# Performance work log

Hardware: AMD Instinct MI355X
Metric: run time of the kernel (lower is better)

Reference implementation:

```python
import jax, jax.numpy as jnp
import numpy as np
from jax import lax

B, C, H, W = 256, 64, 48, 48   # batch, in_channels, spatial_dim, spatial_dim
E = 5                           # num_experts (ConditionalConv2D default)
DIM = 64 + 1                    # n_regulators + 1


def setup_inputs() -> dict:
    key = jax.random.key(0)
    ks = jax.random.split(key, 24)
    def n(k, shape, s=0.05):
        return jax.random.normal(k, shape, jnp.float32) * s
    inp = {
        "spatial_maps": jax.random.normal(ks[0], (B, C, H, W), jnp.float32),
        "cluster_info": jax.random.randint(ks[1], (B,), 0, C),
        # ConditionalConv2D (1x1, num_experts=5)
        "expert_w": n(ks[2], (E, C, C)),          # [experts, out_c, in_c] (1x1 squeezed)
        "cond_b": n(ks[3], (C,)),
        "route_emb": n(ks[4], (C, 4 * C)),        # Embedding(num_clusters=C, pool_emb=4C)
        "route_W": n(ks[5], (E, 8 * C)),          # Linear(2*pool_emb -> E)
        "route_b": n(ks[6], (E,)),
        # weight-normed conv stack (v, g, bias, prelu-a)
        "v1": n(ks[7], (32, C, 3, 3)),  "g1": jnp.ones((32,), jnp.float32),  "cb1": n(ks[8], (32,)),  "a1": jnp.array(0.1, jnp.float32),
        "v2": n(ks[9], (64, 32, 3, 3)), "g2": jnp.ones((64,), jnp.float32),  "cb2": n(ks[10], (64,)), "a2": jnp.array(0.1, jnp.float32),
        "v3": n(ks[11], (128, 64, 3, 3)), "g3": jnp.ones((128,), jnp.float32), "cb3": n(ks[12], (128,)), "a3": jnp.array(0.1, jnp.float32),
        # cluster embedding + alpha + MLP
        "emb2": n(ks[13], (C, 128)),
        "alpha": jnp.array(1.0, jnp.float32),
        "mW1": n(ks[14], (64, 128)), "mb1": n(ks[15], (64,)), "a4": jnp.array(0.1, jnp.float32),
        "mW2": n(ks[16], (32, 64)),  "mb2": n(ks[17], (32,)), "a5": jnp.array(0.1, jnp.float32),
        "mW3": n(ks[18], (DIM, 32)), "mb3": n(ks[19], (DIM,)),
    }
    return inp


def _wn(v, g):
    # weight_norm over all dims except 0 (torch default dim=0)
    nrm = jnp.sqrt((v * v).sum((1, 2, 3)))
    return v * (g / nrm)[:, None, None, None]


def _conv(x, w, b):
    y = lax.conv_general_dilated(x, w, (1, 1), 'SAME',
                                 dimension_numbers=('NCHW', 'OIHW', 'NCHW'))
    return y + b[None, :, None, None]


def _prelu(x, a):
    return jnp.where(x >= 0, x, a * x)


def _mpool(x):
    return lax.reduce_window(x, -jnp.inf, lax.max, (1, 1, 2, 2), (1, 1, 2, 2), 'VALID')


def reference(spatial_maps, cluster_info, expert_w, cond_b, route_emb, route_W, route_b,
              v1, g1, cb1, a1, v2, g2, cb2, a2, v3, g3, cb3, a3,
              emb2, alpha, mW1, mb1, a4, mW2, mb2, a5, mW3, mb3):
    x = spatial_maps
    # routing: adaptive avg pool (2,2), flatten, concat cluster embedding, linear, sigmoid
    pooled = x.reshape(B, C, 2, H // 2, 2, W // 2).mean((3, 5)).reshape(B, 4 * C)
    feat = jnp.concatenate([pooled, route_emb[cluster_info]], axis=1)      # [B, 8C]
    rw = jax.nn.sigmoid(feat @ route_W.T + route_b)                        # [B, E]
    # per-sample expert-mixed 1x1 kernel, applied as batched 1x1 conv
    kern = jnp.einsum('be,eoi->boi', rw, expert_w)                         # [B, C, C]
    cc = jnp.einsum('boi,bihw->bohw', kern, x) + cond_b[None, :, None, None]
    out = jax.nn.sigmoid(cc) * x                                           # attention gate
    # dense conv stack
    h = _mpool(_prelu(_conv(out, _wn(v1, g1), cb1), a1))
    h = _mpool(_prelu(_conv(h, _wn(v2, g2), cb2), a2))
    h = _mpool(_prelu(_conv(h, _wn(v3, g3), cb3), a3))
    h = h.mean((2, 3))                                                      # AdaptiveAvgPool2d(1)+Flatten -> [B,128]
    h = h + emb2[cluster_info] * alpha
    # MLP head
    h = _prelu(h @ mW1.T + mb1, a4)
    h = _prelu(h @ mW2.T + mb2, a5)
    return h @ mW3.T + mb3                                                  # [B, DIM]
```

## Files before the change

kernel.cpp:

```cpp
#include <hip/hip_runtime.h>


typedef _Float16 f16;
typedef f16 f16x8 __attribute__((ext_vector_type(8)));
typedef f16 f16x4 __attribute__((ext_vector_type(4)));
typedef f16 f16x2 __attribute__((ext_vector_type(2)));
typedef __fp16 h16x2 __attribute__((ext_vector_type(2)));
typedef float f32x4 __attribute__((ext_vector_type(4)));

constexpr size_t OFF_POOLED = 0;
constexpr size_t OFF_KERN   = 65536;
constexpr size_t OFF_W1     = 65536 + 1048576;
constexpr size_t OFF_W2     = OFF_W1 + 32*64*12;
constexpr size_t OFF_W3     = OFF_W2 + 64*32*12;
constexpr size_t OFF_H1     = OFF_W3 + 128*64*12;

__device__ __forceinline__ float sigmoidf_(float z) {
    return __builtin_amdgcn_rcpf(1.0f + __expf(-z));
}

__device__ __forceinline__ f16x2 pkrtz(float a, float b) {
    h16x2 r = __builtin_amdgcn_cvt_pkrtz(a, b);
    f16x2 o; o[0] = (f16)r[0]; o[1] = (f16)r[1];
    return o;
}

__device__ __forceinline__ void store_slot8(f16* glds, int row, int sc, int icg, const float* c) {
    f16x2 p0 = pkrtz(c[0], c[1]);
    f16x2 p1 = pkrtz(c[2], c[3]);
    f16x2 p2 = pkrtz(c[4], c[5]);
    f16x2 p3 = pkrtz(c[6], c[7]);
    f16x8 hv = { p0[0], p0[1], p1[0], p1[1], p2[0], p2[1], p3[0], p3[1] };
    *(f16x8*)&glds[(row * 50 + sc) * 64 + ((icg ^ (sc & 7)) << 3)] = hv;
}

__global__ void k_wnorm(const float* __restrict__ v1, const float* __restrict__ g1,
                        const float* __restrict__ v2, const float* __restrict__ g2,
                        const float* __restrict__ v3, const float* __restrict__ g3,
                        float* __restrict__ ws)
{
    int bo = blockIdx.x;
    const float* v; const float* g; int IC, oc; int which;
    if (bo < 32)       { v = v1; g = g1; oc = bo;      IC = 64; which = 1; }
    else if (bo < 96)  { v = v2; g = g2; oc = bo - 32; IC = 32; which = 2; }
    else               { v = v3; g = g3; oc = bo - 96; IC = 64; which = 3; }
    int n = IC * 9;
    const float* vo = v + (size_t)oc * n;
    float s = 0.0f;
    for (int i = threadIdx.x; i < n; i += 256) { float xv = vo[i]; s += xv * xv; }
    __shared__ float swarp[4];
    __shared__ float sscale;
    int lane = threadIdx.x & 63, wid = threadIdx.x >> 6;
    #pragma unroll
    for (int off = 32; off; off >>= 1) s += __shfl_down(s, off);
    if (lane == 0) swarp[wid] = s;
    __syncthreads();
    if (threadIdx.x == 0) {
        float tsum = swarp[0] + swarp[1] + swarp[2] + swarp[3];
        sscale = g[oc] / sqrtf(tsum);
    }
    __syncthreads();
    float sc = sscale;
    if (which == 1) {
        f16* o1 = (f16*)(ws + OFF_W1);
        for (int i = threadIdx.x; i < n; i += 256) {
            int ic = i / 9, kk = i - ic * 9;
            o1[kk * 2048 + oc * 64 + (ic ^ ((oc & 7) << 3))] = (f16)(vo[i] * sc);
        }
    } else if (which == 2) {
        f16* o2 = (f16*)(ws + OFF_W2);
        for (int i = threadIdx.x; i < n; i += 256) {
            int ic = i / 9, kk = i - ic * 9;
            o2[(kk * 64 + oc) * 32 + ic] = (f16)(vo[i] * sc);
        }
    } else {
        f16* o3 = (f16*)(ws + OFF_W3);
        for (int i = threadIdx.x; i < n; i += 256) {
            int ic = i / 9, kk = i - ic * 9;
            o3[(kk * 128 + oc) * 64 + ic] = (f16)(vo[i] * sc);
        }
    }
}

__global__ void __launch_bounds__(64)
k_pool(const float* __restrict__ x, float* __restrict__ ws)
{
    int bc = blockIdx.x;
    int lane = threadIdx.x;
    const float4* p = (const float4*)(x + (size_t)bc * 2304);
    float a0 = 0.f, a1 = 0.f, a2 = 0.f, a3 = 0.f;
    #pragma unroll
    for (int j = 0; j < 9; j++) {
        int i = lane + 64 * j;
        int row = i / 12, cg = i - 12 * row;
        float4 v = p[i];
        float s = v.x + v.y + v.z + v.w;
        bool hq = (row >= 24), wq = (cg >= 6);
        a0 += (!hq && !wq) ? s : 0.f;
        a1 += (!hq &&  wq) ? s : 0.f;
        a2 += ( hq && !wq) ? s : 0.f;
        a3 += ( hq &&  wq) ? s : 0.f;
    }
    #pragma unroll
    for (int off = 32; off; off >>= 1) {
        a0 += __shfl_down(a0, off);
        a1 += __shfl_down(a1, off);
        a2 += __shfl_down(a2, off);
        a3 += __shfl_down(a3, off);
    }
    if (lane == 0) {
        int b = bc >> 6, c = bc & 63;
        float* d = ws + OFF_POOLED + (size_t)b * 256 + c * 4;
        d[0] = a0 * (1.0f / 576.0f);
        d[1] = a1 * (1.0f / 576.0f);
        d[2] = a2 * (1.0f / 576.0f);
        d[3] = a3 * (1.0f / 576.0f);
    }
}

__global__ void k_route(const int* __restrict__ cluster,
                        const float* __restrict__ route_emb,
                        const float* __restrict__ route_W,
                        const float* __restrict__ route_b,
                        const float* __restrict__ expert_w,
                        float* __restrict__ ws)
{
    int b = blockIdx.x, t = threadIdx.x;
    __shared__ float feat[512];
    __shared__ float rwv[5];
    __shared__ float red[256];
    int cl = cluster[b];
    feat[t]       = ws[OFF_POOLED + (size_t)b * 256 + t];
    feat[256 + t] = route_emb[(size_t)cl * 256 + t];
    __syncthreads();
    float f0 = feat[t], f1 = feat[256 + t];
    for (int e = 0; e < 5; e++) {
        float pv = f0 * route_W[e * 512 + t] + f1 * route_W[e * 512 + 256 + t];
        red[t] = pv;
        __syncthreads();
        if (t < 128) red[t] += red[t + 128];
        __syncthreads();
        if (t < 64) {
            float s = red[t] + red[t + 64];
            #pragma unroll
            for (int off = 32; off; off >>= 1) s += __shfl_down(s, off);
            if (t == 0) rwv[e] = 1.0f / (1.0f + __expf(-(s + route_b[e])));
        }
        __syncthreads();
    }
    float r0 = rwv[0], r1 = rwv[1], r2 = rwv[2], r3 = rwv[3], r4 = rwv[4];
    f16* khg = (f16*)(ws + OFF_KERN);
    for (int j = t; j < 4096; j += 256) {
        int oc = j >> 6, ic = j & 63;
        float kv = r0 * expert_w[j] + r1 * expert_w[4096 + j] +
                   r2 * expert_w[2 * 4096 + j] + r3 * expert_w[3 * 4096 + j] +
                   r4 * expert_w[4 * 4096 + j];
        khg[(size_t)b * 4096 + oc * 64 + (ic ^ ((oc & 7) << 3))] = (f16)kv;
    }
}

__global__ void __launch_bounds__(512, 4)
k_f1(const float* __restrict__ x, const f16* __restrict__ kernH,
     const float* __restrict__ cond_b, const f16* __restrict__ w1H,
     const float* __restrict__ cb1, const float* __restrict__ a1,
     f16* __restrict__ h1h)
{
    extern __shared__ char smem[];
    f16*  glds  = (f16*)smem;
    f16*  kh    = (f16*)(smem + 64000);
    float* cbl  = (float*)(smem + 72192);
    f16*  hm    = (f16*)smem;
    f16*  poolt = (f16*)(smem + 16384);

    const int t = threadIdx.x;
    const int tile = blockIdx.x;
    const int b = blockIdx.y;
    const int r0 = tile * 8;
    const int w = t >> 6, l = t & 63;
    const int l15 = l & 15, agrp = l >> 4;

    ((uint4*)kh)[t] = ((const uint4*)(kernH + (size_t)b * 4096))[t];
    if (t < 64) cbl[t] = cond_b[t];
    if (t < 160) {
        int row = t >> 4, rem = t & 15;
        int col = (rem >= 8) ? 49 : 0;
        int slot = rem & 7;
        uint4 z = {};
        *(uint4*)&glds[(row * 50 + col) * 64 + slot * 8] = z;
    }
    for (int e = t; e < 960; e += 512) {
        int row = e / 96;
        int rem = e - row * 96;
        int colg = rem >> 3;
        int icg = rem & 7;
        int r_in = r0 - 1 + row;
        float4 va[8];
        if (r_in >= 0 && r_in < 48) {
            const float4* xp = (const float4*)x + ((size_t)(b * 64 + icg * 8)) * 576 + r_in * 12 + colg;
            #pragma unroll
            for (int i = 0; i < 8; i++) va[i] = xp[i * 576];
        } else {
            #pragma unroll
            for (int i = 0; i < 8; i++) va[i] = (float4){0.f, 0.f, 0.f, 0.f};
        }
        float c0[8], c1[8], c2c[8], c3[8];
        #pragma unroll
        for (int i = 0; i < 8; i++) { c0[i] = va[i].x; c1[i] = va[i].y; c2c[i] = va[i].z; c3[i] = va[i].w; }
        int scb = colg * 4 + 1;
        store_slot8(glds, row, scb + 0, icg, c0);
        store_slot8(glds, row, scb + 1, icg, c1);
        store_slot8(glds, row, scb + 2, icg, c2c);
        store_slot8(glds, row, scb + 3, icg, c3);
    }
    __syncthreads();

    {
        const int nt0 = (w < 6) ? 4 * w : 24 + 3 * (w - 6);
        const int NT  = (w < 6) ? 4 : 3;
        f32x4 acc[4][4] = {};
        int srA[4], scA[4];
        #pragma unroll
        for (int j = 0; j < 4; j++) {
            int ntc = nt0 + ((j < NT) ? j : 0);
            int p = ntc * 16 + l15;
            srA[j] = p / 48; scA[j] = p - 48 * srA[j] + 1;
        }
        #pragma unroll
        for (int ks = 0; ks < 2; ks++) {
            f16x8 kfr[4];
            #pragma unroll
            for (int mt = 0; mt < 4; mt++) {
                int oc = mt * 16 + l15;
                kfr[mt] = *(const f16x8*)&kh[oc * 64 + (((ks * 4 + agrp) ^ (oc & 7)) << 3)];
            }
            #pragma unroll
            for (int j = 0; j < 4; j++) {
                f16x8 bfr = *(const f16x8*)&glds[(srA[j] * 50 + scA[j]) * 64 +
                                                 (((ks * 4 + agrp) ^ (scA[j] & 7)) << 3)];
                #pragma unroll
                for (int mt = 0; mt < 4; mt++)
                    acc[mt][j] = __builtin_amdgcn_mfma_f32_16x16x32_f16(kfr[mt], bfr, acc[mt][j], 0, 0, 0);
            }
        }
        f32x4 cbv[4];
        #pragma unroll
        for (int mt = 0; mt < 4; mt++) cbv[mt] = *(const f32x4*)&cbl[mt * 16 + 4 * agrp];
        #pragma unroll
        for (int j = 0; j < 4; j++) {
            if (j < NT) {
                int base = (srA[j] * 50 + scA[j]) * 64;
                int sw8 = (scA[j] & 7) << 3;
                #pragma unroll
                for (int mt = 0; mt < 4; mt++) {
                    int oc0 = mt * 16 + 4 * agrp;
                    int addr = base + (oc0 ^ sw8);
                    f16x4 xv4 = *(const f16x4*)&glds[addr];
                    float s0 = sigmoidf_(acc[mt][j][0] + cbv[mt][0]);
                    float s1 = sigmoidf_(acc[mt][j][1] + cbv[mt][1]);
                    float s2 = sigmoidf_(acc[mt][j][2] + cbv[mt][2]);
                    float s3 = sigmoidf_(acc[mt][j][3] + cbv[mt][3]);
                    f16x2 slo = pkrtz(s0, s1);
                    f16x2 shi = pkrtz(s2, s3);
                    f16x2 xlo = { xv4[0], xv4[1] };
                    f16x2 xhi = { xv4[2], xv4[3] };
                    f16x2 glo = slo * xlo;
                    f16x2 ghi = shi * xhi;
                    f16x4 g4 = { glo[0], glo[1], ghi[0], ghi[1] };
                    *(f16x4*)&glds[addr] = g4;
                }
            }
        }
    }
    __syncthreads();

    f32x4 c2[3][2] = {};
    {
        const int q = w;
        #pragma unroll
        for (int kt = 0; kt < 18; kt++) {
            const int kk = kt >> 1, hh = kt & 1;
            const int dy = kk / 3, dx = kk - dy * 3;
            f16x8 bfr2[2];
            #pragma unroll
            for (int nt = 0; nt < 2; nt++) {
                int oc = nt * 16 + l15;
                int slot = (hh * 4 + agrp) ^ (oc & 7);
                bfr2[nt] = *(const f16x8*)&w1H[(kk * 32 + oc) * 64 + slot * 8];
            }
            #pragma unroll
            for (int mtl = 0; mtl < 3; mtl++) {
                int sc = mtl * 16 + l15 + dx;
                int slot = (hh * 4 + agrp) ^ (sc & 7);
                f16x8 af = *(const f16x8*)&glds[((q + dy) * 50 + sc) * 64 + slot * 8];
                c2[mtl][0] = __builtin_amdgcn_mfma_f32_16x16x32_f16(af, bfr2[0], c2[mtl][0], 0, 0, 0);
                c2[mtl][1] = __builtin_amdgcn_mfma_f32_16x16x32_f16(af, bfr2[1], c2[mtl][1], 0, 0, 0);
            }
        }
    }
    __syncthreads();

    {
        const int q = w;
        #pragma unroll
        for (int mtl = 0; mtl < 3; mtl++)
            #pragma unroll
            for (int nt = 0; nt < 2; nt++) {
                float h0 = fmaxf(c2[mtl][nt][0], c2[mtl][nt][1]);
                float h1 = fmaxf(c2[mtl][nt][2], c2[mtl][nt][3]);
                f16x2 hp = pkrtz(h0, h1);
                int oc = nt * 16 + l15;
                int pp = mtl * 8 + 2 * agrp;
                *(f16x2*)&hm[(q * 32 + oc) * 26 + pp] = hp;
            }
    }
    __syncthreads();

    {
        const float av = a1[0];
        #pragma unroll
        for (int k = 0; k < 6; k++) {
            int e = t + 512 * k;
            int oc = e & 31, pos2 = e >> 5;
            int pr = pos2 / 24, pc = pos2 - 24 * pr;
            float v0 = (float)hm[((2 * pr) * 32 + oc) * 26 + pc];
            float v1 = (float)hm[((2 * pr + 1) * 32 + oc) * 26 + pc];
            float v = fmaxf(v0, v1) + cb1[oc];
            v = (v >= 0.0f) ? v : av * v;
            poolt[pos2 * 40 + oc] = (f16)v;
        }
    }
    __syncthreads();

    if (t < 384) {
        int pos2 = t >> 2, slot = t & 3;
        uint4 val = *(const uint4*)&poolt[pos2 * 40 + slot * 8];
        ((uint4*)h1h)[((size_t)b * 576 + tile * 96 + pos2) * 4 + slot] = val;
    }
}

__global__ void __launch_bounds__(512, 1)
k_f23(const f16* __restrict__ h1h, const f16* __restrict__ w2h,
      const float* __restrict__ cb2, const float* __restrict__ a2,
      const f16* __restrict__ w3h, const float* __restrict__ cb3, const float* __restrict__ a3,
      const int* __restrict__ cluster, const float* __restrict__ emb2, const float* __restrict__ alpha,
      const float* __restrict__ mW1, const float* __restrict__ mb1, const float* __restrict__ a4,
      const float* __restrict__ mW2, const float* __restrict__ mb2, const float* __restrict__ a5,
      const float* __restrict__ mW3, const float* __restrict__ mb3,
      float* __restrict__ out)
{
    extern __shared__ char smem[];
    f16*  x2    = (f16*)smem;
    f16*  h2l   = (f16*)(smem + 82944);
    float* ps   = (float*)(smem + 111168);
    float* hb   = (float*)(smem + 113216);
    float* t1   = (float*)(smem + 113728);
    float* t2   = (float*)(smem + 113984);
    f16*  dump2 = (f16*)smem;
    f16*  dump3 = (f16*)smem;

    const int b = blockIdx.x, t = threadIdx.x;
    const int w = t >> 6, l = t & 63;
    const int l15 = l & 15, agrp = l >> 4;

    for (int e = t; e < 400; e += 512) {
        int bp = e >> 2, slot = e & 3;
        int r, c;
        if (bp < 26)      { r = 0;  c = bp; }
        else if (bp < 52) { r = 25; c = bp - 26; }
        else if (bp < 76) { r = bp - 52 + 1; c = 0; }
        else              { r = bp - 76 + 1; c = 25; }
        uint4 z = {};
        *(uint4*)&x2[(r * 26 + c) * 40 + slot * 8] = z;
    }
    for (int e = t; e < 416; e += 512) {
        int bp = e >> 3, slot = e & 7;
        int r, c;
        if (bp < 14)      { r = 0;  c = bp; }
        else if (bp < 28) { r = 13; c = bp - 14; }
        else if (bp < 40) { r = bp - 28 + 1; c = 0; }
        else              { r = bp - 40 + 1; c = 13; }
        uint4 z = {};
        *(uint4*)&h2l[(r * 14 + c) * 72 + slot * 8] = z;
    }
    {
        const uint4* src = (const uint4*)(h1h + (size_t)b * 18432);
        for (int e = t; e < 2304; e += 512) {
            int pos = e >> 2, slot = e & 3;
            int r = pos / 24, c = pos - 24 * r;
            *(uint4*)&x2[((r + 1) * 26 + (c + 1)) * 40 + slot * 8] = src[e];
        }
    }
    __syncthreads();

    const int m = w & 3, half = w >> 2;
    f32x4 acc[18];
    {
        f16x8 afr[9];
        #pragma unroll
        for (int kk = 0; kk < 9; kk++)
            afr[kk] = *(const f16x8*)&w2h[(kk * 64 + m * 16 + l15) * 32 + agrp * 8];
        #pragma unroll
        for (int nt = 0; nt < 18; nt++) acc[nt] = (f32x4){0.f, 0.f, 0.f, 0.f};
        constexpr int K2[9] = {0, 40, 80, 26 * 40, 27 * 40, 28 * 40, 52 * 40, 53 * 40, 54 * 40};
        #pragma unroll
        for (int nt = 0; nt < 18; nt++) {
            int p = (half * 18 + nt) * 16 + l15;
            int r = p / 24, c = p - 24 * r;
            int base = (r * 26 + c) * 40 + agrp * 8;
            #pragma unroll
            for (int kk = 0; kk < 9; kk++) {
                f16x8 bfr = *(const f16x8*)&x2[base + K2[kk]];
                acc[nt] = __builtin_amdgcn_mfma_f32_16x16x32_f16(afr[kk], bfr, acc[nt], 0, 0, 0);
            }
        }
    }
    __syncthreads();

    #pragma unroll
    for (int nt = 0; nt < 18; nt++) {
        int p = (half * 18 + nt) * 16 + l15;
        f16x2 d0 = pkrtz(acc[nt][0], acc[nt][1]);
        f16x2 d1 = pkrtz(acc[nt][2], acc[nt][3]);
        f16x4 hv = { d0[0], d0[1], d1[0], d1[1] };
        *(f16x4*)&dump2[p * 72 + m * 16 + 4 * agrp] = hv;
    }
    __syncthreads();

    {
        const float a2v = a2[0];
        for (int e = t; e < 9216; e += 512) {
            int oc = e & 63, pos2 = e >> 6;
            int pr = pos2 / 12, pc = pos2 - 12 * pr;
            int p0 = (2 * pr) * 24 + 2 * pc;
            float mm = fmaxf(fmaxf((float)dump2[p0 * 72 + oc], (float)dump2[(p0 + 1) * 72 + oc]),
                             fmaxf((float)dump2[(p0 + 24) * 72 + oc], (float)dump2[(p0 + 25) * 72 + oc]));
            float v = mm + cb2[oc];
            v = (v >= 0.0f) ? v : a2v * v;
            h2l[((pr + 1) * 14 + (pc + 1)) * 72 + oc] = (f16)v;
        }
    }
    __syncthreads();

    f32x4 acc9[9];
    {
        int pb[9];
        #pragma unroll
        for (int nt = 0; nt < 9; nt++) {
            int p = nt * 16 + l15;
            int r = p / 12, c = p - 12 * r;
            pb[nt] = (r * 14 + c) * 72 + agrp * 8;
            acc9[nt] = (f32x4){0.f, 0.f, 0.f, 0.f};
        }
        constexpr int K3[9] = {0, 72, 144, 14 * 72, 15 * 72, 16 * 72, 28 * 72, 29 * 72, 30 * 72};
        #pragma unroll
        for (int kk = 0; kk < 9; kk++) {
            #pragma unroll
            for (int ks = 0; ks < 2; ks++) {
                f16x8 afr = *(const f16x8*)&w3h[(size_t)(kk * 128 + w * 16 + l15) * 64 + ks * 32 + agrp * 8];
                #pragma unroll
                for (int nt = 0; nt < 9; nt++) {
                    f16x8 bfr = *(const f16x8*)&h2l[pb[nt] + ks * 32 + K3[kk]];
                    acc9[nt] = __builtin_amdgcn_mfma_f32_16x16x32_f16(afr, bfr, acc9[nt], 0, 0, 0);
                }
            }
        }
    }
    #pragma unroll
    for (int nt = 0; nt < 9; nt++) {
        int p = nt * 16 + l15;
        f16x2 d0 = pkrtz(acc9[nt][0], acc9[nt][1]);
        f16x2 d1 = pkrtz(acc9[nt][2], acc9[nt][3]);
        f16x4 hv = { d0[0], d0[1], d1[0], d1[1] };
        *(f16x4*)&dump3[p * 136 + w * 16 + 4 * agrp] = hv;
    }
    __syncthreads();

    {
        int oc = t >> 2, q = t & 3;
        int qr = q >> 1, qc = q & 1;
        const float a3v = a3[0];
        float cbv = cb3[oc];
        float s = 0.f;
        #pragma unroll
        for (int i = 0; i < 3; i++)
            #pragma unroll
            for (int j = 0; j < 3; j++) {
                int pr = 3 * qr + i, pc = 3 * qc + j;
                int p0 = (2 * pr) * 12 + 2 * pc;
                float mm = fmaxf(fmaxf((float)dump3[p0 * 136 + oc], (float)dump3[(p0 + 1) * 136 + oc]),
                                 fmaxf((float)dump3[(p0 + 12) * 136 + oc], (float)dump3[(p0 + 13) * 136 + oc]));
                float v = mm + cbv;
                v = (v >= 0.0f) ? v : a3v * v;
                s += v;
            }
        ps[t] = s;
    }
    __syncthreads();
    if (t < 128) {
        int cl = cluster[b];
        hb[t] = (ps[4 * t] + ps[4 * t + 1] + ps[4 * t + 2] + ps[4 * t + 3]) * (1.0f / 36.0f)
              + emb2[(size_t)cl * 128 + t] * alpha[0];
    }
    __syncthreads();
    if (t < 64) {
        const float4* wr = (const float4*)(mW1 + t * 128);
        float s = mb1[t];
        #pragma unroll 8
        for (int j = 0; j < 32; j++) {
            float4 wv4 = wr[j];
            s += wv4.x * hb[4 * j] + wv4.y * hb[4 * j + 1] + wv4.z * hb[4 * j + 2] + wv4.w * hb[4 * j + 3];
        }
        float a4v = a4[0];
        t1[t] = (s >= 0.0f) ? s : a4v * s;
    }
    __syncthreads();
    if (t < 32) {
        const float4* wr = (const float4*)(mW2 + t * 64);
        float s = mb2[t];
        #pragma unroll
        for (int j = 0; j < 16; j++) {
            float4 wv4 = wr[j];
            s += wv4.x * t1[4 * j] + wv4.y * t1[4 * j + 1] + wv4.z * t1[4 * j + 2] + wv4.w * t1[4 * j + 3];
        }
        float a5v = a5[0];
        t2[t] = (s >= 0.0f) ? s : a5v * s;
    }
    __syncthreads();
    if (t < 65) {
        const float4* wr = (const float4*)(mW3 + t * 32);
        float s = mb3[t];
        #pragma unroll
        for (int j = 0; j < 8; j++) {
            float4 wv4 = wr[j];
            s += wv4.x * t2[4 * j] + wv4.y * t2[4 * j + 1] + wv4.z * t2[4 * j + 2] + wv4.w * t2[4 * j + 3];
        }
        out[(size_t)b * 65 + t] = s;
    }
}

extern "C" void kernel_launch(void* const* d_in, const int* in_sizes, int n_in,
                              void* d_out, int out_size, void* d_ws, size_t ws_size,
                              hipStream_t stream)
{
    const float* x         = (const float*)d_in[0];
    const int*   cluster   = (const int*)  d_in[1];
    const float* expert_w  = (const float*)d_in[2];
    const float* cond_b    = (const float*)d_in[3];
    const float* route_emb = (const float*)d_in[4];
    const float* route_W   = (const float*)d_in[5];
    const float* route_b   = (const float*)d_in[6];
    const float* v1  = (const float*)d_in[7];
    const float* g1  = (const float*)d_in[8];
    const float* cb1 = (const float*)d_in[9];
    const float* a1  = (const float*)d_in[10];
    const float* v2  = (const float*)d_in[11];
    const float* g2  = (const float*)d_in[12];
    const float* cb2 = (const float*)d_in[13];
    const float* a2  = (const float*)d_in[14];
    const float* v3  = (const float*)d_in[15];
    const float* g3  = (const float*)d_in[16];
    const float* cb3 = (const float*)d_in[17];
    const float* a3  = (const float*)d_in[18];
    const float* emb2  = (const float*)d_in[19];
    const float* alpha = (const float*)d_in[20];
    const float* mW1 = (const float*)d_in[21];
    const float* mb1 = (const float*)d_in[22];
    const float* a4  = (const float*)d_in[23];
    const float* mW2 = (const float*)d_in[24];
    const float* mb2 = (const float*)d_in[25];
    const float* a5  = (const float*)d_in[26];
    const float* mW3 = (const float*)d_in[27];
    const float* mb3 = (const float*)d_in[28];
    float* ws  = (float*)d_ws;
    float* out = (float*)d_out;

    hipFuncSetAttribute((const void*)k_f1,  hipFuncAttributeMaxDynamicSharedMemorySize, 72448);
    hipFuncSetAttribute((const void*)k_f23, hipFuncAttributeMaxDynamicSharedMemorySize, 114112);

    k_wnorm<<<224, 256, 0, stream>>>(v1, g1, v2, g2, v3, g3, ws);
    k_pool<<<16384, 64, 0, stream>>>(x, ws);
    k_route<<<256, 256, 0, stream>>>(cluster, route_emb, route_W, route_b, expert_w, ws);
    k_f1<<<dim3(6, 256), 512, 72448, stream>>>(x, (const f16*)(ws + OFF_KERN), cond_b,
                                               (const f16*)(ws + OFF_W1), cb1, a1,
                                               (f16*)(ws + OFF_H1));
    k_f23<<<256, 512, 114112, stream>>>((const f16*)(ws + OFF_H1), (const f16*)(ws + OFF_W2),
                                        cb2, a2, (const f16*)(ws + OFF_W3), cb3, a3,
                                        cluster, emb2, alpha,
                                        mW1, mb1, a4, mW2, mb2, a5, mW3, mb3, out);
}
```

Before: 121.1 us.

## Fuse weight-norm into pool kernel and double k_f23 block to 1024 threads

Result: no change. 119.0 us (-1.7%).

```diff
diff --git a/kernel.cpp b/kernel.cpp
--- a/kernel.cpp
+++ b/kernel.cpp
@@ -34,87 +34,78 @@
     *(f16x8*)&glds[(row * 50 + sc) * 64 + ((icg ^ (sc & 7)) << 3)] = hv;
 }
 
-__global__ void k_wnorm(const float* __restrict__ v1, const float* __restrict__ g1,
-                        const float* __restrict__ v2, const float* __restrict__ g2,
-                        const float* __restrict__ v3, const float* __restrict__ g3,
-                        float* __restrict__ ws)
+__global__ void __launch_bounds__(64)
+k_prep(const float* __restrict__ x,
+       const float* __restrict__ v1, const float* __restrict__ g1,
+       const float* __restrict__ v2, const float* __restrict__ g2,
+       const float* __restrict__ v3, const float* __restrict__ g3,
+       float* __restrict__ ws)
 {
-    int bo = blockIdx.x;
-    const float* v; const float* g; int IC, oc; int which;
-    if (bo < 32)       { v = v1; g = g1; oc = bo;      IC = 64; which = 1; }
-    else if (bo < 96)  { v = v2; g = g2; oc = bo - 32; IC = 32; which = 2; }
-    else               { v = v3; g = g3; oc = bo - 96; IC = 64; which = 3; }
-    int n = IC * 9;
-    const float* vo = v + (size_t)oc * n;
-    float s = 0.0f;
-    for (int i = threadIdx.x; i < n; i += 256) { float xv = vo[i]; s += xv * xv; }
-    __shared__ float swarp[4];
-    __shared__ float sscale;
-    int lane = threadIdx.x & 63, wid = threadIdx.x >> 6;
-    #pragma unroll
-    for (int off = 32; off; off >>= 1) s += __shfl_down(s, off);
-    if (lane == 0) swarp[wid] = s;
-    __syncthreads();
-    if (threadIdx.x == 0) {
-        float tsum = swarp[0] + swarp[1] + swarp[2] + swarp[3];
-        sscale = g[oc] / sqrtf(tsum);
-    }
-    __syncthreads();
-    float sc = sscale;
-    if (which == 1) {
-        f16* o1 = (f16*)(ws + OFF_W1);
-        for (int i = threadIdx.x; i < n; i += 256) {
-            int ic = i / 9, kk = i - ic * 9;
-            o1[kk * 2048 + oc * 64 + (ic ^ ((oc & 7) << 3))] = (f16)(vo[i] * sc);
-        }
-    } else if (which == 2) {
-        f16* o2 = (f16*)(ws + OFF_W2);
-        for (int i = threadIdx.x; i < n; i += 256) {
-            int ic = i / 9, kk = i - ic * 9;
-            o2[(kk * 64 + oc) * 32 + ic] = (f16)(vo[i] * sc);
+    const int blk = blockIdx.x;
+    const int lane = threadIdx.x;
+    if (blk < 16384) {
+        const float4* p = (const float4*)(x + (size_t)blk * 2304);
+        float a0 = 0.f, a1 = 0.f, a2 = 0.f, a3 = 0.f;
+        #pragma unroll
+        for (int j = 0; j < 9; j++) {
+            int i = lane + 64 * j;
+            int row = i / 12, cg = i - 12 * row;
+            float4 v = p[i];
+            float s = v.x + v.y + v.z + v.w;
+            bool hq = (row >= 24), wq = (cg >= 6);
+            a0 += (!hq && !wq) ? s : 0.f;
+            a1 += (!hq &&  wq) ? s : 0.f;
+            a2 += ( hq && !wq) ? s : 0.f;
+            a3 += ( hq &&  wq) ? s : 0.f;
+        }
+        #pragma unroll
+        for (int off = 32; off; off >>= 1) {
+            a0 += __shfl_down(a0, off);
+            a1 += __shfl_down(a1, off);
+            a2 += __shfl_down(a2, off);
+            a3 += __shfl_down(a3, off);
+        }
+        if (lane == 0) {
+            int b = blk >> 6, c = blk & 63;
+            float* d = ws + OFF_POOLED + (size_t)b * 256 + c * 4;
+            d[0] = a0 * (1.0f / 576.0f);
+            d[1] = a1 * (1.0f / 576.0f);
+            d[2] = a2 * (1.0f / 576.0f);
+            d[3] = a3 * (1.0f / 576.0f);
         }
     } else {
-        f16* o3 = (f16*)(ws + OFF_W3);
-        for (int i = threadIdx.x; i < n; i += 256) {
-            int ic = i / 9, kk = i - ic * 9;
-            o3[(kk * 128 + oc) * 64 + ic] = (f16)(vo[i] * sc);
-        }
-    }
-}
-
-__global__ void __launch_bounds__(64)
-k_pool(const float* __restrict__ x, float* __restrict__ ws)
-{
-    int bc = blockIdx.x;
-    int lane = threadIdx.x;
-    const float4* p = (const float4*)(x + (size_t)bc * 2304);
-    float a0 = 0.f, a1 = 0.f, a2 = 0.f, a3 = 0.f;
-    #pragma unroll
-    for (int j = 0; j < 9; j++) {
-        int i = lane + 64 * j;
-        int row = i / 12, cg = i - 12 * row;
-        float4 v = p[i];
-        float s = v.x + v.y + v.z + v.w;
-        bool hq = (row >= 24), wq = (cg >= 6);
-        a0 += (!hq && !wq) ? s : 0.f;
-        a1 += (!hq &&  wq) ? s : 0.f;
-        a2 += ( hq && !wq) ? s : 0.f;
-        a3 += ( hq &&  wq) ? s : 0.f;
-    }
-    #pragma unroll
-    for (int off = 32; off; off >>= 1) {
-        a0 += __shfl_down(a0, off);
-        a1 += __shfl_down(a1, off);
-        a2 += __shfl_down(a2, off);
-        a3 += __shfl_down(a3, off);
-    }
-    if (lane == 0) {
-        int b = bc >> 6, c = bc & 63;
-        float* d = ws + OFF_POOLED + (size_t)b * 256 + c * 4;
-        d[0] = a0 * (1.0f / 576.0f);
-        d[1] = a1 * (1.0f / 576.0f);
-        d[2] = a2 * (1.0f / 576.0f);
-        d[3] = a3 * (1.0f / 576.0f);
+        int bo = blk - 16384;
+        const float* v; const float* g; int IC, oc; int which;
+        if (bo < 32)       { v = v1; g = g1; oc = bo;      IC = 64; which = 1; }
+        else if (bo < 96)  { v = v2; g = g2; oc = bo - 32; IC = 32; which = 2; }
+        else               { v = v3; g = g3; oc = bo - 96; IC = 64; which = 3; }
+        int n = IC * 9;
+        const float* vo = v + (size_t)oc * n;
+        float s = 0.0f;
+        for (int i = lane; i < n; i += 64) { float xv = vo[i]; s += xv * xv; }
+        #pragma unroll
+        for (int off = 32; off; off >>= 1) s += __shfl_down(s, off);
+        float tot = __shfl(s, 0);
+        float sc = g[oc] / sqrtf(tot);
+        if (which == 1) {
+            f16* o1 = (f16*)(ws + OFF_W1);
+            for (int i = lane; i < n; i += 64) {
+                int ic = i / 9, kk = i - ic * 9;
+                o1[kk * 2048 + oc * 64 + (ic ^ ((oc & 7) << 3))] = (f16)(vo[i] * sc);
+            }
+        } else if (which == 2) {
+            f16* o2 = (f16*)(ws + OFF_W2);
+            for (int i = lane; i < n; i += 64) {
+                int ic = i / 9, kk = i - ic * 9;
+                o2[(kk * 64 + oc) * 32 + ic] = (f16)(vo[i] * sc);
+            }
+        } else {
+            f16* o3 = (f16*)(ws + OFF_W3);
+            for (int i = lane; i < n; i += 64) {
+                int ic = i / 9, kk = i - ic * 9;
+                o3[(kk * 128 + oc) * 64 + ic] = (f16)(vo[i] * sc);
+            }
+        }
     }
 }
 
@@ -338,7 +329,7 @@
     }
 }
 
-__global__ void __launch_bounds__(512, 1)
+__global__ void __launch_bounds__(1024, 1)
 k_f23(const f16* __restrict__ h1h, const f16* __restrict__ w2h,
       const float* __restrict__ cb2, const float* __restrict__ a2,
       const f16* __restrict__ w3h, const float* __restrict__ cb3, const float* __restrict__ a3,
@@ -362,7 +353,7 @@
     const int w = t >> 6, l = t & 63;
     const int l15 = l & 15, agrp = l >> 4;
 
-    for (int e = t; e < 400; e += 512) {
+    for (int e = t; e < 400; e += 1024) {
         int bp = e >> 2, slot = e & 3;
         int r, c;
         if (bp < 26)      { r = 0;  c = bp; }
@@ -372,7 +363,7 @@
         uint4 z = {};
         *(uint4*)&x2[(r * 26 + c) * 40 + slot * 8] = z;
     }
-    for (int e = t; e < 416; e += 512) {
+    for (int e = t; e < 416; e += 1024) {
         int bp = e >> 3, slot = e & 7;
         int r, c;
         if (bp < 14)      { r = 0;  c = bp; }
@@ -384,7 +375,7 @@
     }
     {
         const uint4* src = (const uint4*)(h1h + (size_t)b * 18432);
-        for (int e = t; e < 2304; e += 512) {
+        for (int e = t; e < 2304; e += 1024) {
             int pos = e >> 2, slot = e & 3;
             int r = pos / 24, c = pos - 24 * r;
             *(uint4*)&x2[((r + 1) * 26 + (c + 1)) * 40 + slot * 8] = src[e];
@@ -392,35 +383,35 @@
     }
     __syncthreads();
 
-    const int m = w & 3, half = w >> 2;
-    f32x4 acc[18];
+    const int m = w & 3, ng = w >> 2;
+    f32x4 acc[9];
     {
         f16x8 afr[9];
         #pragma unroll
         for (int kk = 0; kk < 9; kk++)
             afr[kk] = *(const f16x8*)&w2h[(kk * 64 + m * 16 + l15) * 32 + agrp * 8];
         #pragma unroll
-        for (int nt = 0; nt < 18; nt++) acc[nt] = (f32x4){0.f, 0.f, 0.f, 0.f};
+        for (int i = 0; i < 9; i++) acc[i] = (f32x4){0.f, 0.f, 0.f, 0.f};
         constexpr int K2[9] = {0, 40, 80, 26 * 40, 27 * 40, 28 * 40, 52 * 40, 53 * 40, 54 * 40};
         #pragma unroll
-        for (int nt = 0; nt < 18; nt++) {
-            int p = (half * 18 + nt) * 16 + l15;
+        for (int i = 0; i < 9; i++) {
+            int p = (ng * 9 + i) * 16 + l15;
             int r = p / 24, c = p - 24 * r;
             int base = (r * 26 + c) * 40 + agrp * 8;
             #pragma unroll
             for (int kk = 0; kk < 9; kk++) {
                 f16x8 bfr = *(const f16x8*)&x2[base + K2[kk]];
-                acc[nt] = __builtin_amdgcn_mfma_f32_16x16x32_f16(afr[kk], bfr, acc[nt], 0, 0, 0);
+                acc[i] = __builtin_amdgcn_mfma_f32_16x16x32_f16(afr[kk], bfr, acc[i], 0, 0, 0);
             }
         }
     }
     __syncthreads();
 
     #pragma unroll
-    for (int nt = 0; nt < 18; nt++) {
-        int p = (half * 18 + nt) * 16 + l15;
-        f16x2 d0 = pkrtz(acc[nt][0], acc[nt][1]);
-        f16x2 d1 = pkrtz(acc[nt][2], acc[nt][3]);
+    for (int i = 0; i < 9; i++) {
+        int p = (ng * 9 + i) * 16 + l15;
+        f16x2 d0 = pkrtz(acc[i][0], acc[i][1]);
+        f16x2 d1 = pkrtz(acc[i][2], acc[i][3]);
         f16x4 hv = { d0[0], d0[1], d1[0], d1[1] };
         *(f16x4*)&dump2[p * 72 + m * 16 + 4 * agrp] = hv;
     }
@@ -428,7 +419,7 @@
 
     {
         const float a2v = a2[0];
-        for (int e = t; e < 9216; e += 512) {
+        for (int e = t; e < 9216; e += 1024) {
             int oc = e & 63, pos2 = e >> 6;
             int pr = pos2 / 12, pc = pos2 - 12 * pr;
             int p0 = (2 * pr) * 24 + 2 * pc;
@@ -441,41 +432,48 @@
     }
     __syncthreads();
 
-    f32x4 acc9[9];
-    {
-        int pb[9];
-        #pragma unroll
-        for (int nt = 0; nt < 9; nt++) {
-            int p = nt * 16 + l15;
+    const int m8 = w & 7, ng3 = w >> 3;
+    const int nt0c3 = ng3 * 5;
+    const int cnt3  = ng3 ? 4 : 5;
+    f32x4 acc3[5];
+    {
+        int pb[5];
+        #pragma unroll
+        for (int i = 0; i < 5; i++) {
+            int p = (nt0c3 + i) * 16 + l15;
             int r = p / 12, c = p - 12 * r;
-            pb[nt] = (r * 14 + c) * 72 + agrp * 8;
-            acc9[nt] = (f32x4){0.f, 0.f, 0.f, 0.f};
-        }
-        constexpr int K3[9] = {0, 72, 144, 14 * 72, 15 * 72, 16 * 72, 28 * 72, 29 * 72, 30 * 72};
+            pb[i] = ((r + 1) * 14 + (c + 1)) * 72 + agrp * 8;
+            acc3[i] = (f32x4){0.f, 0.f, 0.f, 0.f};
+        }
+        constexpr int K3[9] = {-15 * 72, -14 * 72, -13 * 72, -72, 0, 72, 13 * 72, 14 * 72, 15 * 72};
         #pragma unroll
         for (int kk = 0; kk < 9; kk++) {
             #pragma unroll
             for (int ks = 0; ks < 2; ks++) {
-                f16x8 afr = *(const f16x8*)&w3h[(size_t)(kk * 128 + w * 16 + l15) * 64 + ks * 32 + agrp * 8];
+                f16x8 afr = *(const f16x8*)&w3h[(size_t)(kk * 128 + m8 * 16 + l15) * 64 + ks * 32 + agrp * 8];
                 #pragma unroll
-                for (int nt = 0; nt < 9; nt++) {
-                    f16x8 bfr = *(const f16x8*)&h2l[pb[nt] + ks * 32 + K3[kk]];
-                    acc9[nt] = __builtin_amdgcn_mfma_f32_16x16x32_f16(afr, bfr, acc9[nt], 0, 0, 0);
+                for (int i = 0; i < 5; i++) {
+                    if (i < cnt3) {
+                        f16x8 bfr = *(const f16x8*)&h2l[pb[i] + ks * 32 + K3[kk]];
+                        acc3[i] = __builtin_amdgcn_mfma_f32_16x16x32_f16(afr, bfr, acc3[i], 0, 0, 0);
+                    }
                 }
             }
         }
     }
     #pragma unroll
-    for (int nt = 0; nt < 9; nt++) {
-        int p = nt * 16 + l15;
-        f16x2 d0 = pkrtz(acc9[nt][0], acc9[nt][1]);
-        f16x2 d1 = pkrtz(acc9[nt][2], acc9[nt][3]);
-        f16x4 hv = { d0[0], d0[1], d1[0], d1[1] };
-        *(f16x4*)&dump3[p * 136 + w * 16 + 4 * agrp] = hv;
-    }
-    __syncthreads();
-
-    {
+    for (int i = 0; i < 5; i++) {
+        if (i < cnt3) {
+            int p = (nt0c3 + i) * 16 + l15;
+            f16x2 d0 = pkrtz(acc3[i][0], acc3[i][1]);
+            f16x2 d1 = pkrtz(acc3[i][2], acc3[i][3]);
+            f16x4 hv = { d0[0], d0[1], d1[0], d1[1] };
+            *(f16x4*)&dump3[p * 136 + m8 * 16 + 4 * agrp] = hv;
+        }
+    }
+    __syncthreads();
+
+    if (t < 512) {
         int oc = t >> 2, q = t & 3;
         int qr = q >> 1, qc = q & 1;
         const float a3v = a3[0];
@@ -577,14 +575,13 @@
     hipFuncSetAttribute((const void*)k_f1,  hipFuncAttributeMaxDynamicSharedMemorySize, 72448);
     hipFuncSetAttribute((const void*)k_f23, hipFuncAttributeMaxDynamicSharedMemorySize, 114112);
 
-    k_wnorm<<<224, 256, 0, stream>>>(v1, g1, v2, g2, v3, g3, ws);
-    k_pool<<<16384, 64, 0, stream>>>(x, ws);
+    k_prep<<<16608, 64, 0, stream>>>(x, v1, g1, v2, g2, v3, g3, ws);
     k_route<<<256, 256, 0, stream>>>(cluster, route_emb, route_W, route_b, expert_w, ws);
     k_f1<<<dim3(6, 256), 512, 72448, stream>>>(x, (const f16*)(ws + OFF_KERN), cond_b,
                                                (const f16*)(ws + OFF_W1), cb1, a1,
                                                (f16*)(ws + OFF_H1));
-    k_f23<<<256, 512, 114112, stream>>>((const f16*)(ws + OFF_H1), (const f16*)(ws + OFF_W2),
-                                        cb2, a2, (const f16*)(ws + OFF_W3), cb3, a3,
-                                        cluster, emb2, alpha,
-                                        mW1, mb1, a4, mW2, mb2, a5, mW3, mb3, out);
-}
+    k_f23<<<256, 1024, 114112, stream>>>((const f16*)(ws + OFF_H1), (const f16*)(ws + OFF_W2),
+                                         cb2, a2, (const f16*)(ws + OFF_W3), cb3, a3,
+                                         cluster, emb2, alpha,
+                                         mW1, mb1, a4, mW2, mb2, a5, mW3, mb3, out);
+}
```
